# Performance work log

Measured on AMD Instinct MI355X. Metric: run time of the kernel, lower is better.

Reference implementation:

```python
import jax, jax.numpy as jnp
import numpy as np

N_NODES, N_EDGES, N_GRAPHS = 5000, 80000, 64
LATENT, HID, STEPS = 128, 512, 3


def _mlp(h, Ws, bs):
    # MLP: ReLU after every linear (incl. last) -- MLPwoLastAct is the variant without it
    for W, b in zip(Ws, bs):
        h = jax.nn.relu(h @ W + b)
    return h


def _mlp_wo_last_act(h, Ws, bs):
    n = len(Ws)
    for i, (W, b) in enumerate(zip(Ws, bs)):
        h = h @ W + b
        if i < n - 1:
            h = jax.nn.relu(h)
    return h


def setup_inputs() -> dict:
    key = jax.random.key(0)
    ks = iter(jax.random.split(key, 64))

    def nrm(shape, s=0.05):
        return (jax.random.normal(next(ks), shape) * s).astype(jnp.float32)

    inp = {}
    inp["x"] = jax.random.normal(next(ks), (N_NODES, LATENT), jnp.float32)
    inp["edge_index"] = jax.random.randint(next(ks), (2, N_EDGES), 0, N_NODES, jnp.int32)
    inp["edge_attr"] = jax.random.normal(next(ks), (N_EDGES, LATENT), jnp.float32)
    inp["u"] = jax.random.normal(next(ks), (N_GRAPHS, LATENT), jnp.float32)
    inp["node_batch"] = jnp.sort(jax.random.randint(next(ks), (N_NODES,), 0, N_GRAPHS, jnp.int32))
    inp["edge_batch"] = jnp.sort(jax.random.randint(next(ks), (N_EDGES,), 0, N_GRAPHS, jnp.int32))
    inp["pos"] = jax.random.normal(next(ks), (N_NODES, 3), jnp.float32)
    inp["last_pos_init"] = jax.random.uniform(next(ks), (N_NODES, 3), jnp.float32, -1.0, 1.0)

    # PosEmbeddingwithMask: pos MLP(3->128->128), dis MLP(1->128->128)
    inp["pos_emb_W1"], inp["pos_emb_b1"] = nrm((3, LATENT)), nrm((LATENT,))
    inp["pos_emb_W2"], inp["pos_emb_b2"] = nrm((LATENT, LATENT)), nrm((LATENT,))
    inp["dis_W1"], inp["dis_b1"] = nrm((1, LATENT)), nrm((LATENT,))
    inp["dis_W2"], inp["dis_b2"] = nrm((LATENT, LATENT)), nrm((LATENT,))

    # per-layer edge / node MLPs: (4*latent) -> 512 -> 512 -> 128, stacked over STEPS
    cin = 4 * LATENT
    for pre in ("edge", "node"):
        inp[f"{pre}_W1"], inp[f"{pre}_b1"] = nrm((STEPS, cin, HID)), nrm((STEPS, HID))
        inp[f"{pre}_W2"], inp[f"{pre}_b2"] = nrm((STEPS, HID, HID)), nrm((STEPS, HID))
        inp[f"{pre}_W3"], inp[f"{pre}_b3"] = nrm((STEPS, HID, LATENT)), nrm((STEPS, LATENT))

    # global MLP only for layers 0..STEPS-2: (3*latent) -> 512 -> 512 -> 128
    gL, gin = STEPS - 1, 3 * LATENT
    inp["glob_W1"], inp["glob_b1"] = nrm((gL, gin, HID)), nrm((gL, HID))
    inp["glob_W2"], inp["glob_b2"] = nrm((gL, HID, HID)), nrm((gL, HID))
    inp["glob_W3"], inp["glob_b3"] = nrm((gL, HID, LATENT)), nrm((gL, LATENT))

    # shared pos_decoder: MLPwoLastAct(128 -> 128 -> 3)
    inp["dec_W1"], inp["dec_b1"] = nrm((LATENT, LATENT)), nrm((LATENT,))
    inp["dec_W2"], inp["dec_b2"] = nrm((LATENT, 3)), nrm((3,))
    return inp


def reference(x, edge_index, edge_attr, u, node_batch, edge_batch, pos, last_pos_init,
              pos_emb_W1, pos_emb_b1, pos_emb_W2, pos_emb_b2,
              dis_W1, dis_b1, dis_W2, dis_b2,
              edge_W1, edge_b1, edge_W2, edge_b2, edge_W3, edge_b3,
              node_W1, node_b1, node_W2, node_b2, node_W3, node_b3,
              glob_W1, glob_b1, glob_W2, glob_b2, glob_W3, glob_b3,
              dec_W1, dec_b1, dec_W2, dec_b2):
    src, dst = edge_index[0], edge_index[1]
    N = x.shape[0]
    counts = jnp.maximum(
        jax.ops.segment_sum(jnp.ones((N, 1), x.dtype), node_batch, N_GRAPHS), 1.0)

    def move2origin(p):
        mean = jax.ops.segment_sum(p, node_batch, N_GRAPHS) / counts
        return p - mean[node_batch]

    xs, es, us = x, edge_attr, u
    last_pos = last_pos_init  # pos_new_zeros.uniform_(-1, 1), materialized as input
    pos_preds = []
    for l in range(STEPS):
        p = last_pos  # mode='mol2conf': pos = last_pred
        # PosEmbeddingwithMask
        ex = xs + _mlp(p, (pos_emb_W1, pos_emb_W2), (pos_emb_b1, pos_emb_b2))
        length = jnp.linalg.norm(p[src] - p[dst], axis=-1, keepdims=True)  # [E,1]
        ee = es + _mlp(length, (dis_W1, dis_W2), (dis_b1, dis_b2))
        # edge update: gather -> MLP
        edge_in = jnp.concatenate([ex[src], ex[dst], ee, us[edge_batch]], axis=-1)
        e1 = _mlp(edge_in, (edge_W1[l], edge_W2[l], edge_W3[l]),
                  (edge_b1[l], edge_b2[l], edge_b3[l]))
        # scatter-reduce (sum) to nodes, then node MLP
        sent = jax.ops.segment_sum(e1, src, N)
        recv = jax.ops.segment_sum(e1, dst, N)
        node_in = jnp.concatenate([ex, sent, recv, us[node_batch]], axis=-1)
        x1 = _mlp(node_in, (node_W1[l], node_W2[l], node_W3[l]),
                  (node_b1[l], node_b2[l], node_b3[l]))
        # global update (None on last layer)
        if l < STEPS - 1:
            g_in = jnp.concatenate([us,
                                    jax.ops.segment_sum(x1, node_batch, N_GRAPHS),
                                    jax.ops.segment_sum(e1, edge_batch, N_GRAPHS)], axis=-1)
            u1 = _mlp(g_in, (glob_W1[l], glob_W2[l], glob_W3[l]),
                      (glob_b1[l], glob_b2[l], glob_b3[l]))
        else:
            u1 = us
        # residuals (dropout is identity in eval)
        xs, es, us = x1 + xs, e1 + es, u1 + us
        # pred_pos_residual=True
        delta = _mlp_wo_last_act(xs, (dec_W1, dec_W2), (dec_b1, dec_b2))
        last_pos = move2origin(last_pos + delta)
        pos_preds.append(last_pos)
    return xs, es, us, jnp.stack(pos_preds)
```

## Files before the change

kernel.cpp:

```cpp
#include <hip/hip_runtime.h>
#include <hip/hip_bf16.h>
#include <stdint.h>

#define NN 5000
#define NE 80000
#define NG 64
#define LAT 128
#define HIDN 512

typedef __hip_bfloat16 bf16;
typedef short short8 __attribute__((ext_vector_type(8)));
typedef float f32x4 __attribute__((ext_vector_type(4)));

__device__ __forceinline__ float b2f(bf16 v) { return __bfloat162float(v); }
__device__ __forceinline__ bf16 f2b(float v) { return __float2bfloat16(v); }
__device__ __forceinline__ short f2bs(float v) {
    bf16 b = __float2bfloat16(v);
    short s; __builtin_memcpy(&s, &b, 2); return s;
}

template<int MODE>
__global__ __launch_bounds__(256, 4)
void gemm64_kernel(const bf16* __restrict__ A, const bf16* __restrict__ Bt,
                   const float* __restrict__ bias,
                   const float* residf, const bf16* residb,
                   float* out_sf, bf16* out_sb, bf16* out_rb,
                   int M, int N, int nnt,
                   const int* __restrict__ g_src, const int* __restrict__ g_dst,
                   const int* __restrict__ g_eb,
                   const bf16* __restrict__ g_ex, const bf16* __restrict__ g_ee,
                   const bf16* __restrict__ g_us)
{
    constexpr int K = 512, NT = K / 64;
    __shared__ __align__(16) char lds[24576];

    const int tid  = threadIdx.x;
    const int lane = tid & 63;
    const int w    = tid >> 6;
    const int li   = lane & 15, grp = lane >> 4;
    const int wr   = w >> 1, wc = w & 1;

    const int nb  = gridDim.x;
    const int q   = nb >> 3, r = nb & 7;
    const int xcd = blockIdx.x & 7, jj = blockIdx.x >> 3;
    const int wg  = (xcd < r ? xcd * (q + 1) : r * (q + 1) + (xcd - r) * q) + jj;
    const int m0  = (wg / nnt) * 128;
    const int n0  = (wg % nnt) * 64;

    f32x4 acc[4][2];
#pragma unroll
    for (int m = 0; m < 4; ++m)
#pragma unroll
        for (int n = 0; n < 2; ++n)
            acc[m][n] = (f32x4){0.f, 0.f, 0.f, 0.f};

    int he[4], hs[4], hd[4], hb[4];
    if (MODE == 1) {
#pragma unroll
        for (int c = 0; c < 4; ++c) {
            const int p  = (tid + c * 256) * 16;
            const int qb = p ^ ((p >> 3) & 0x70);
            int e = m0 + (qb >> 7); if (e >= M) e = M - 1;
            he[c] = e;
            hs[c] = g_src[e]; hd[c] = g_dst[e]; hb[c] = g_eb[e];
        }
    }

    char* ldsA = lds;
    char* ldsB = lds + 16384;

    for (int t = 0; t < NT; ++t) {
#pragma unroll
        for (int c = 0; c < 4; ++c) {
            const int p  = (tid + c * 256) * 16;
            const int qb = p ^ ((p >> 3) & 0x70);
            const int row = qb >> 7;
            const int kk  = (qb & 127) >> 1;
            const bf16* srcp;
            if (MODE == 1) {
                const int seg = t >> 1;
                const int so  = ((t & 1) << 6) + kk;
                if (seg == 0)      srcp = g_ex + (size_t)hs[c] * LAT + so;
                else if (seg == 1) srcp = g_ex + (size_t)hd[c] * LAT + so;
                else if (seg == 2) srcp = g_ee + (size_t)he[c] * LAT + so;
                else               srcp = g_us + (size_t)hb[c] * LAT + so;
            } else {
                int rr = m0 + row; if (rr >= M) rr = M - 1;
                srcp = A + (size_t)rr * K + t * 64 + kk;
            }
            __builtin_amdgcn_global_load_lds(
                (__attribute__((address_space(1))) const void*)srcp,
                (__attribute__((address_space(3))) void*)(ldsA + p), 16, 0, 0);
        }
#pragma unroll
        for (int c = 0; c < 2; ++c) {
            const int p  = (tid + c * 256) * 16;
            const int qb = p ^ ((p >> 3) & 0x70);
            const int row = qb >> 7;
            const int kk  = (qb & 127) >> 1;
            const bf16* srcp = Bt + (size_t)(n0 + row) * K + t * 64 + kk;
            __builtin_amdgcn_global_load_lds(
                (__attribute__((address_space(1))) const void*)srcp,
                (__attribute__((address_space(3))) void*)(ldsB + p), 16, 0, 0);
        }
        __syncthreads();

        short8 af[4][2], bf[2][2];
#pragma unroll
        for (int m = 0; m < 4; ++m) {
            const int row = wr * 64 + m * 16 + li;
            const int xr  = (row & 7) << 4;
#pragma unroll
            for (int s = 0; s < 2; ++s)
                af[m][s] = *(const short8*)(ldsA +
                    ((row * 128 + s * 64 + grp * 16) ^ xr));
        }
#pragma unroll
        for (int n = 0; n < 2; ++n) {
            const int row = wc * 32 + n * 16 + li;
            const int xr  = (row & 7) << 4;
#pragma unroll
            for (int s = 0; s < 2; ++s)
                bf[n][s] = *(const short8*)(ldsB +
                    ((row * 128 + s * 64 + grp * 16) ^ xr));
        }
#pragma unroll
        for (int m = 0; m < 4; ++m)
#pragma unroll
            for (int n = 0; n < 2; ++n)
#pragma unroll
                for (int s = 0; s < 2; ++s)
                    acc[m][n] = __builtin_amdgcn_mfma_f32_16x16x32_bf16(
                        af[m][s], bf[n][s], acc[m][n], 0, 0, 0);
        __syncthreads();
    }

#pragma unroll
    for (int m = 0; m < 4; ++m) {
        const int growb = m0 + wr * 64 + m * 16 + grp * 4;
#pragma unroll
        for (int n = 0; n < 2; ++n) {
            const int gcol = n0 + wc * 32 + n * 16 + li;
            const float bv = bias[gcol];
#pragma unroll
            for (int j = 0; j < 4; ++j) {
                const int grow = growb + j;
                if (grow >= M) continue;
                float val = fmaxf(acc[m][n][j] + bv, 0.f);
                const size_t oo = (size_t)grow * N + gcol;
                if (out_rb) out_rb[oo] = f2b(val);
                float sum = val;
                if (residf) sum += residf[oo];
                if (residb) sum += b2f(residb[oo]);
                if (out_sf) out_sf[oo] = sum;
                if (out_sb) out_sb[oo] = f2b(sum);
            }
        }
    }
}

template<int K, int MODE>
__global__ __launch_bounds__(256)
void gemm_kernel(const bf16* __restrict__ A,
                 const bf16* __restrict__ Bt,
                 const float* __restrict__ bias,
                 const float* residf, const bf16* residb,
                 float* out_sf, bf16* out_sb, bf16* out_rb,
                 int M, int N, int nnt,
                 const int* __restrict__ g_src, const int* __restrict__ g_dst,
                 const float* __restrict__ lp,
                 const float* __restrict__ aW, const float* __restrict__ ab)
{
    constexpr bool HASA = (MODE == 0);
    __shared__ __align__(16) bf16 As[HASA ? 128 * 32 : 8];
    __shared__ __align__(16) bf16 Bs[128 * 32];
    const int tid  = threadIdx.x;
    const int lane = tid & 63;
    const int w    = tid >> 6;
    const int li   = lane & 15, grp = lane >> 4;
    const int wr   = w >> 1, wc = w & 1;

    const int nb  = gridDim.x;
    const int q   = nb >> 3, r = nb & 7;
    const int xcd = blockIdx.x & 7, jj = blockIdx.x >> 3;
    const int wg  = (xcd < r ? xcd * (q + 1) : r * (q + 1) + (xcd - r) * q) + jj;
    const int m0  = (wg / nnt) * 128;
    const int n0  = (wg % nnt) * 128;

    f32x4 acc[4][4];
#pragma unroll
    for (int m = 0; m < 4; ++m)
#pragma unroll
        for (int n = 0; n < 4; ++n)
            acc[m][n] = (f32x4){0.f, 0.f, 0.f, 0.f};

    float r0[4], r1[4], r2[4];
    if (MODE == 2) {
#pragma unroll
        for (int m = 0; m < 4; ++m) {
            int rr = m0 + wr * 64 + m * 16 + li; if (rr >= M) rr = M - 1;
            r0[m] = lp[rr * 3 + 0]; r1[m] = lp[rr * 3 + 1]; r2[m] = lp[rr * 3 + 2];
        }
    } else if (MODE == 3) {
#pragma unroll
        for (int m = 0; m < 4; ++m) {
            int rr = m0 + wr * 64 + m * 16 + li; if (rr >= M) rr = M - 1;
            const int s = g_src[rr], d = g_dst[rr];
            const float dx = lp[s*3+0] - lp[d*3+0];
            const float dy = lp[s*3+1] - lp[d*3+1];
            const float dz = lp[s*3+2] - lp[d*3+2];
            r0[m] = sqrtf(dx*dx + dy*dy + dz*dz);
        }
    }

    const int offBase = w * 1024 + lane * 16;

    for (int kt = 0; kt < K / 32; ++kt) {
        if (HASA) {
#pragma unroll
            for (int c = 0; c < 2; ++c) {
                const int off = offBase + c * 4096;
                const int rr_ = off >> 6;
                const int g   = (off >> 4) & 3;
                const int gl  = g ^ ((rr_ >> 1) & 3);
                int rr = m0 + rr_; if (rr >= M) rr = M - 1;
                const bf16* srcp = A + (size_t)rr * K + kt * 32 + gl * 8;
                __builtin_amdgcn_global_load_lds(
                    (__attribute__((address_space(1))) const void*)srcp,
                    (__attribute__((address_space(3))) void*)((char*)As + off),
                    16, 0, 0);
            }
        }
#pragma unroll
        for (int c = 0; c < 2; ++c) {
            const int off = offBase + c * 4096;
            const int rr_ = off >> 6;
            const int g   = (off >> 4) & 3;
            const int gl  = g ^ ((rr_ >> 1) & 3);
            const bf16* srcp = Bt + (size_t)(n0 + rr_) * K + kt * 32 + gl * 8;
            __builtin_amdgcn_global_load_lds(
                (__attribute__((address_space(1))) const void*)srcp,
                (__attribute__((address_space(3))) void*)((char*)Bs + off),
                16, 0, 0);
        }
        __syncthreads();

        short8 af[4], bfr[4];
        if (HASA) {
#pragma unroll
            for (int m = 0; m < 4; ++m) {
                const int rr_  = wr * 64 + m * 16 + li;
                const int boff = rr_ * 64 + ((grp * 16) ^ (((rr_ >> 1) & 3) << 4));
                af[m] = *(const short8*)((const char*)As + boff);
            }
        } else {
            const int kk0 = kt * 32 + grp * 8;
            float bb[8], w0[8], w1[8], w2[8];
            *(f32x4*)&bb[0] = *(const f32x4*)(ab + kk0);
            *(f32x4*)&bb[4] = *(const f32x4*)(ab + kk0 + 4);
            *(f32x4*)&w0[0] = *(const f32x4*)(aW + kk0);
            *(f32x4*)&w0[4] = *(const f32x4*)(aW + kk0 + 4);
            if (MODE == 2) {
                *(f32x4*)&w1[0] = *(const f32x4*)(aW + K + kk0);
                *(f32x4*)&w1[4] = *(const f32x4*)(aW + K + kk0 + 4);
                *(f32x4*)&w2[0] = *(const f32x4*)(aW + 2 * K + kk0);
                *(f32x4*)&w2[4] = *(const f32x4*)(aW + 2 * K + kk0 + 4);
            }
#pragma unroll
            for (int m = 0; m < 4; ++m) {
                short8 v;
#pragma unroll
                for (int e = 0; e < 8; ++e) {
                    float s;
                    if (MODE == 2)
                        s = bb[e] + r0[m]*w0[e] + r1[m]*w1[e] + r2[m]*w2[e];
                    else
                        s = bb[e] + r0[m]*w0[e];
                    v[e] = f2bs(fmaxf(s, 0.f));
                }
                af[m] = v;
            }
        }
#pragma unroll
        for (int n = 0; n < 4; ++n) {
            const int rr_  = wc * 64 + n * 16 + li;
            const int boff = rr_ * 64 + ((grp * 16) ^ (((rr_ >> 1) & 3) << 4));
            bfr[n] = *(const short8*)((const char*)Bs + boff);
        }
#pragma unroll
        for (int m = 0; m < 4; ++m)
#pragma unroll
            for (int n = 0; n < 4; ++n)
                acc[m][n] = __builtin_amdgcn_mfma_f32_16x16x32_bf16(
                    af[m], bfr[n], acc[m][n], 0, 0, 0);
        __syncthreads();
    }

#pragma unroll
    for (int m = 0; m < 4; ++m) {
        const int growb = m0 + wr * 64 + m * 16 + grp * 4;
#pragma unroll
        for (int n = 0; n < 4; ++n) {
            const int gcol = n0 + wc * 64 + n * 16 + li;
            const float bv = bias[gcol];
#pragma unroll
            for (int j = 0; j < 4; ++j) {
                const int grow = growb + j;
                if (grow >= M) continue;
                float val = fmaxf(acc[m][n][j] + bv, 0.f);
                const size_t oo = (size_t)grow * N + gcol;
                if (out_rb) out_rb[oo] = f2b(val);
                float sum = val;
                if (residf) sum += residf[oo];
                if (residb) sum += b2f(residb[oo]);
                if (out_sf) out_sf[oo] = sum;
                if (out_sb) out_sb[oo] = f2b(sum);
            }
        }
    }
}

struct TDesc { const float* src; bf16* dst; int K, N, nblk, nb32; };
struct TPack { TDesc d[28]; int n; };

__global__ __launch_bounds__(256)
void transpose_kernel(TPack p)
{
    __shared__ float t[32][33];
    int b = blockIdx.x, mi = 0;
    while (mi < p.n && b >= p.d[mi].nblk) { b -= p.d[mi].nblk; ++mi; }
    if (mi >= p.n) return;
    TDesc d = p.d[mi];
    const int kb = b / d.nb32, nb = b % d.nb32;
    const int k0 = kb * 32, n0 = nb * 32;
    const int tx = threadIdx.x & 31, ty = threadIdx.x >> 5;
#pragma unroll
    for (int qq = 0; qq < 4; ++qq) {
        const int kk = ty + qq * 8;
        t[kk][tx] = d.src[(size_t)(k0 + kk) * d.N + n0 + tx];
    }
    __syncthreads();
#pragma unroll
    for (int qq = 0; qq < 4; ++qq) {
        const int nn = ty + qq * 8;
        d.dst[(size_t)(n0 + nn) * d.K + k0 + tx] = f2b(t[tx][nn]);
    }
}

__global__ void deg_kernel(const int* __restrict__ idx, int n, int* deg)
{
    int e = blockIdx.x * 256 + threadIdx.x;
    if (e < n) atomicAdd(&deg[idx[e]], 1);
}

__global__ __launch_bounds__(256)
void scan_kernel(const int* __restrict__ deg, int* __restrict__ offs, int n)
{
    __shared__ int tot[256];
    const int t = threadIdx.x;
    const int per = (n + 255) / 256;
    const int b = t * per;
    int s = 0;
    for (int i = 0; i < per; ++i) if (b + i < n) s += deg[b + i];
    tot[t] = s;
    __syncthreads();
    for (int d = 1; d < 256; d <<= 1) {
        int v = (t >= d) ? tot[t - d] : 0;
        __syncthreads();
        tot[t] += v;
        __syncthreads();
    }
    int excl = (t == 0) ? 0 : tot[t - 1];
    for (int i = 0; i < per; ++i)
        if (b + i < n) { offs[b + i] = excl; excl += deg[b + i]; }
    if (t == 255) offs[n] = tot[255];
}

__global__ void perm_kernel(const int* __restrict__ idx, int n,
                            int* cursor, int* __restrict__ perm)
{
    int e = blockIdx.x * 256 + threadIdx.x;
    if (e < n) { int p = atomicAdd(&cursor[idx[e]], 1); perm[p] = e; }
}

__global__ __launch_bounds__(128)
void node_in_kernel(const bf16* __restrict__ exb, const bf16* __restrict__ e1f,
                    const bf16* __restrict__ usb, const int* __restrict__ nbat,
                    const int* __restrict__ offs_s, const int* __restrict__ perm_s,
                    const int* __restrict__ offs_d, const int* __restrict__ perm_d,
                    bf16* __restrict__ node_in)
{
    const int i = blockIdx.x;
    const int c = threadIdx.x;
    float s1 = 0.f, s2 = 0.f;
    const int s_lo = offs_s[i], s_hi = offs_s[i + 1];
    for (int j = s_lo; j < s_hi; ++j)
        s1 += b2f(e1f[(size_t)perm_s[j] * LAT + c]);
    const int d_lo = offs_d[i], d_hi = offs_d[i + 1];
    for (int j = d_lo; j < d_hi; ++j)
        s2 += b2f(e1f[(size_t)perm_d[j] * LAT + c]);
    const size_t o = (size_t)i * (4 * LAT);
    node_in[o + c]           = exb[(size_t)i * LAT + c];
    node_in[o + LAT + c]     = f2b(s1);
    node_in[o + 2 * LAT + c] = f2b(s2);
    node_in[o + 3 * LAT + c] = usb[(size_t)nbat[i] * LAT + c];
}

__global__ __launch_bounds__(128)
void seg_reduce_kernel(const bf16* __restrict__ vals, const int* __restrict__ batch,
                       float* out, int R, int rows_per_block)
{
    const int r0 = blockIdx.x * rows_per_block;
    if (r0 >= R) return;
    const int c = threadIdx.x;
    const int r1 = min(r0 + rows_per_block, R);
    int g = batch[r0];
    float s = 0.f;
    for (int r = r0; r < r1; ++r) {
        const int gb = batch[r];
        if (gb != g) {
            atomicAdd(&out[(size_t)g * LAT + c], s);
            g = gb; s = 0.f;
        }
        s += b2f(vals[(size_t)r * LAT + c]);
    }
    atomicAdd(&out[(size_t)g * LAT + c], s);
}

__global__ void build_g_in_kernel(const float* __restrict__ us,
                                  const float* __restrict__ gx,
                                  const float* __restrict__ ge,
                                  bf16* __restrict__ out)
{
    int id = blockIdx.x * 256 + threadIdx.x;
    if (id >= NG * 384) return;
    int g = id / 384, c = id % 384;
    int seg = c >> 7, c7 = c & 127;
    float v;
    if (seg == 0)      v = us[g * LAT + c7];
    else if (seg == 1) v = gx[g * LAT + c7];
    else               v = ge[g * LAT + c7];
    out[id] = f2b(v);
}

__global__ void counts_kernel(const int* __restrict__ nbat, float* counts)
{
    int id = blockIdx.x * 256 + threadIdx.x;
    if (id < NN) atomicAdd(&counts[nbat[id]], 1.0f);
}

__global__ void cvt_kernel(const float* __restrict__ in, bf16* __restrict__ out, int n)
{
    int id = blockIdx.x * 256 + threadIdx.x;
    if (id < n) out[id] = f2b(in[id]);
}

__global__ void us_double_kernel(float* us)
{
    int id = blockIdx.x * 256 + threadIdx.x;
    if (id < NG * LAT) us[id] *= 2.0f;
}

__global__ __launch_bounds__(64)
void dec2_kernel(const bf16* __restrict__ dh, const float* __restrict__ W2,
                 const float* __restrict__ b2, const float* __restrict__ lp,
                 const int* __restrict__ nbat, float* __restrict__ ptmp, float* psum)
{
    int i = blockIdx.x;
    int l = threadIdx.x;
    float a0 = 0.f, a1 = 0.f, a2 = 0.f;
#pragma unroll
    for (int q = 0; q < 2; ++q) {
        int k = l + q * 64;
        float h = b2f(dh[i * LAT + k]);
        a0 += h * W2[k * 3 + 0];
        a1 += h * W2[k * 3 + 1];
        a2 += h * W2[k * 3 + 2];
    }
#pragma unroll
    for (int off = 32; off > 0; off >>= 1) {
        a0 += __shfl_down(a0, off, 64);
        a1 += __shfl_down(a1, off, 64);
        a2 += __shfl_down(a2, off, 64);
    }
    if (l == 0) {
        int g = nbat[i];
        float p0 = lp[i*3+0] + a0 + b2[0];
        float p1 = lp[i*3+1] + a1 + b2[1];
        float p2 = lp[i*3+2] + a2 + b2[2];
        ptmp[i*3+0] = p0; ptmp[i*3+1] = p1; ptmp[i*3+2] = p2;
        atomicAdd(&psum[g*3+0], p0);
        atomicAdd(&psum[g*3+1], p1);
        atomicAdd(&psum[g*3+2], p2);
    }
}

__global__ void finalize_pos_kernel(const float* __restrict__ ptmp,
                                    const float* __restrict__ psum,
                                    const float* __restrict__ counts,
                                    const int* __restrict__ nbat,
                                    float* __restrict__ lp, float* __restrict__ pos_out)
{
    int id = blockIdx.x * 256 + threadIdx.x;
    if (id >= NN * 3) return;
    int i = id / 3, d = id % 3;
    int g = nbat[i];
    float v = ptmp[id] - psum[g*3+d] / fmaxf(counts[g], 1.f);
    lp[id] = v;
    pos_out[id] = v;
}

extern "C" void kernel_launch(void* const* d_in, const int* in_sizes, int n_in,
                              void* d_out, int out_size, void* d_ws, size_t ws_size,
                              hipStream_t stream)
{
    const float* x        = (const float*)d_in[0];
    const int*   ei       = (const int*)d_in[1];
    const int*   src      = ei;
    const int*   dst      = ei + NE;
    const float* eattr    = (const float*)d_in[2];
    const float* u        = (const float*)d_in[3];
    const int*   nbat     = (const int*)d_in[4];
    const int*   ebat     = (const int*)d_in[5];
    const float* lp_init  = (const float*)d_in[7];
    const float* pW1 = (const float*)d_in[8];  const float* pb1 = (const float*)d_in[9];
    const float* pW2 = (const float*)d_in[10]; const float* pb2 = (const float*)d_in[11];
    const float* dW1 = (const float*)d_in[12]; const float* db1 = (const float*)d_in[13];
    const float* dW2 = (const float*)d_in[14]; const float* db2 = (const float*)d_in[15];
    const float* eW1 = (const float*)d_in[16]; const float* eb1 = (const float*)d_in[17];
    const float* eW2 = (const float*)d_in[18]; const float* eb2 = (const float*)d_in[19];
    const float* eW3 = (const float*)d_in[20]; const float* eb3 = (const float*)d_in[21];
    const float* nW1 = (const float*)d_in[22]; const float* nb1 = (const float*)d_in[23];
    const float* nW2 = (const float*)d_in[24]; const float* nb2 = (const float*)d_in[25];
    const float* nW3 = (const float*)d_in[26]; const float* nb3 = (const float*)d_in[27];
    const float* gW1 = (const float*)d_in[28]; const float* gb1 = (const float*)d_in[29];
    const float* gW2 = (const float*)d_in[30]; const float* gb2 = (const float*)d_in[31];
    const float* gW3 = (const float*)d_in[32]; const float* gb3 = (const float*)d_in[33];
    const float* dcW1 = (const float*)d_in[34]; const float* dcb1 = (const float*)d_in[35];
    const float* dcW2 = (const float*)d_in[36]; const float* dcb2 = (const float*)d_in[37];

    float* xs = (float*)d_out;
    float* es = xs + (size_t)NN * LAT;
    float* us = es + (size_t)NE * LAT;
    float* pos_out = us + (size_t)NG * LAT;

    char* wp = (char*)d_ws;
    auto alloc = [&](size_t nbytes) {
        void* r = (void*)wp;
        wp += (nbytes + 255) & ~(size_t)255;
        return r;
    };
    bf16* eW1t = (bf16*)alloc((size_t)3*512*512*2);
    bf16* eW2t = (bf16*)alloc((size_t)3*512*512*2);
    bf16* eW3t = (bf16*)alloc((size_t)3*128*512*2);
    bf16* nW1t = (bf16*)alloc((size_t)3*512*512*2);
    bf16* nW2t = (bf16*)alloc((size_t)3*512*512*2);
    bf16* nW3t = (bf16*)alloc((size_t)3*128*512*2);
    bf16* gW1t = (bf16*)alloc((size_t)2*512*384*2);
    bf16* gW2t = (bf16*)alloc((size_t)2*512*512*2);
    bf16* gW3t = (bf16*)alloc((size_t)2*128*512*2);
    bf16* pW2t = (bf16*)alloc((size_t)128*128*2);
    bf16* dW2t = (bf16*)alloc((size_t)128*128*2);
    bf16* dcW1t = (bf16*)alloc((size_t)128*128*2);
    bf16* exb  = (bf16*)alloc((size_t)NN*LAT*2);
    bf16* usb  = (bf16*)alloc((size_t)NG*LAT*2);
    bf16* esb  = (bf16*)alloc((size_t)NE*LAT*2);
    bf16* eeb  = (bf16*)alloc((size_t)NE*LAT*2);
    bf16* h1   = (bf16*)alloc((size_t)NE*HIDN*2);
    bf16* h2   = (bf16*)alloc((size_t)NE*HIDN*2);
    bf16* e1f  = (bf16*)alloc((size_t)NE*LAT*2);
    bf16* x1f  = (bf16*)alloc((size_t)NN*LAT*2);
    float* gx  = (float*)alloc((size_t)NG*LAT*4);
    float* ge  = (float*)alloc((size_t)NG*LAT*4);
    bf16* node_in = (bf16*)alloc((size_t)NN*HIDN*2);
    bf16* nh1  = (bf16*)alloc((size_t)NN*HIDN*2);
    bf16* nh2  = (bf16*)alloc((size_t)NN*HIDN*2);
    bf16* xsb  = (bf16*)alloc((size_t)NN*LAT*2);
    bf16* g_in = (bf16*)alloc((size_t)NG*384*2);
    bf16* gh1  = (bf16*)alloc((size_t)NG*HIDN*2);
    bf16* gh2  = (bf16*)alloc((size_t)NG*HIDN*2);
    bf16* dh   = (bf16*)alloc((size_t)NN*LAT*2);
    float* lp   = (float*)alloc((size_t)NN*3*4);
    float* ptmp = (float*)alloc((size_t)NN*3*4);
    float* psum = (float*)alloc((size_t)NG*3*4);
    float* counts = (float*)alloc((size_t)NG*4);
    int* deg    = (int*)alloc((size_t)NN*4);
    int* offs_s = (int*)alloc((size_t)(NN+1)*4);
    int* offs_d = (int*)alloc((size_t)(NN+1)*4);
    int* cur_s  = (int*)alloc((size_t)NN*4);
    int* cur_d  = (int*)alloc((size_t)NN*4);
    int* perm_s = (int*)alloc((size_t)NE*4);
    int* perm_d = (int*)alloc((size_t)NE*4);

    hipMemcpyAsync(xs, x,     (size_t)NN*LAT*4, hipMemcpyDeviceToDevice, stream);
    hipMemcpyAsync(us, u,     (size_t)NG*LAT*4, hipMemcpyDeviceToDevice, stream);
    hipMemcpyAsync(lp, lp_init, (size_t)NN*3*4, hipMemcpyDeviceToDevice, stream);
    hipMemsetAsync(counts, 0, NG*4, stream);
    counts_kernel<<<(NN+255)/256, 256, 0, stream>>>(nbat, counts);
    cvt_kernel<<<(NG*LAT+255)/256, 256, 0, stream>>>(us, usb, NG*LAT);
    cvt_kernel<<<(NE*LAT+255)/256, 256, 0, stream>>>(eattr, esb, NE*LAT);

    const int eb256 = (NE + 255) / 256;
    hipMemsetAsync(deg, 0, NN*4, stream);
    deg_kernel<<<eb256, 256, 0, stream>>>(src, NE, deg);
    scan_kernel<<<1, 256, 0, stream>>>(deg, offs_s, NN);
    hipMemsetAsync(deg, 0, NN*4, stream);
    deg_kernel<<<eb256, 256, 0, stream>>>(dst, NE, deg);
    scan_kernel<<<1, 256, 0, stream>>>(deg, offs_d, NN);
    hipMemcpyAsync(cur_s, offs_s, NN*4, hipMemcpyDeviceToDevice, stream);
    hipMemcpyAsync(cur_d, offs_d, NN*4, hipMemcpyDeviceToDevice, stream);
    perm_kernel<<<eb256, 256, 0, stream>>>(src, NE, cur_s, perm_s);
    perm_kernel<<<eb256, 256, 0, stream>>>(dst, NE, cur_d, perm_d);

    TPack pk{}; int nd = 0, totb = 0;
    auto addT = [&](const float* s, bf16* d, int K, int N) {
        pk.d[nd].src = s; pk.d[nd].dst = d; pk.d[nd].K = K; pk.d[nd].N = N;
        pk.d[nd].nblk = (K/32)*(N/32); pk.d[nd].nb32 = N/32;
        totb += pk.d[nd].nblk; ++nd;
    };
    for (int l = 0; l < 3; ++l) {
        addT(eW1 + (size_t)l*512*512, eW1t + (size_t)l*512*512, 512, 512);
        addT(eW2 + (size_t)l*512*512, eW2t + (size_t)l*512*512, 512, 512);
        addT(eW3 + (size_t)l*512*128, eW3t + (size_t)l*128*512, 512, 128);
        addT(nW1 + (size_t)l*512*512, nW1t + (size_t)l*512*512, 512, 512);
        addT(nW2 + (size_t)l*512*512, nW2t + (size_t)l*512*512, 512, 512);
        addT(nW3 + (size_t)l*512*128, nW3t + (size_t)l*128*512, 512, 128);
    }
    for (int l = 0; l < 2; ++l) {
        addT(gW1 + (size_t)l*384*512, gW1t + (size_t)l*512*384, 384, 512);
        addT(gW2 + (size_t)l*512*512, gW2t + (size_t)l*512*512, 512, 512);
        addT(gW3 + (size_t)l*512*128, gW3t + (size_t)l*128*512, 512, 128);
    }
    addT(pW2, pW2t, 128, 128);
    addT(dW2, dW2t, 128, 128);
    addT(dcW1, dcW1t, 128, 128);
    pk.n = nd;
    transpose_kernel<<<totb, 256, 0, stream>>>(pk);

    const int mtE  = NE / 128;
    const int mtN  = (NN + 127) / 128;
    #define NIL3 nullptr, nullptr, nullptr

    for (int l = 0; l < 3; ++l) {
        gemm_kernel<128,2><<<mtN, 256, 0, stream>>>(
            nullptr, pW2t, pb2, xs, nullptr, nullptr, exb, nullptr, NN, LAT, 1,
            nullptr, nullptr, lp, pW1, pb1);
        gemm_kernel<128,3><<<mtE, 256, 0, stream>>>(
            nullptr, dW2t, db2, nullptr, esb, nullptr, eeb, nullptr, NE, LAT, 1,
            src, dst, lp, dW1, db1);
        gemm64_kernel<1><<<mtE*8, 256, 0, stream>>>(
            nullptr, eW1t + (size_t)l*512*512, eb1 + l*HIDN, nullptr, nullptr,
            nullptr, nullptr, h1, NE, HIDN, 8,
            src, dst, ebat, exb, eeb, usb);
        gemm64_kernel<0><<<mtE*8, 256, 0, stream>>>(
            h1, eW2t + (size_t)l*512*512, eb2 + l*HIDN, nullptr, nullptr,
            nullptr, nullptr, h2, NE, HIDN, 8, NIL3, NIL3);
        gemm64_kernel<0><<<mtE*2, 256, 0, stream>>>(
            h2, eW3t + (size_t)l*128*512, eb3 + l*LAT, nullptr, esb,
            (l == 2 ? es : nullptr), (l < 2 ? esb : nullptr), e1f, NE, LAT, 2,
            NIL3, NIL3);
        if (l < 2) {
            hipMemsetAsync(gx, 0, (size_t)2*NG*LAT*4, stream);
            seg_reduce_kernel<<<(NE+63)/64, 128, 0, stream>>>(e1f, ebat, ge, NE, 64);
        }
        node_in_kernel<<<NN, 128, 0, stream>>>(
            exb, e1f, usb, nbat, offs_s, perm_s, offs_d, perm_d, node_in);
        gemm64_kernel<0><<<mtN*8, 256, 0, stream>>>(
            node_in, nW1t + (size_t)l*512*512, nb1 + l*HIDN, nullptr, nullptr,
            nullptr, nullptr, nh1, NN, HIDN, 8, NIL3, NIL3);
        gemm64_kernel<0><<<mtN*8, 256, 0, stream>>>(
            nh1, nW2t + (size_t)l*512*512, nb2 + l*HIDN, nullptr, nullptr,
            nullptr, nullptr, nh2, NN, HIDN, 8, NIL3, NIL3);
        gemm64_kernel<0><<<mtN*2, 256, 0, stream>>>(
            nh2, nW3t + (size_t)l*128*512, nb3 + l*LAT, xs, nullptr,
            xs, xsb, x1f, NN, LAT, 2, NIL3, NIL3);
        if (l < 2) {
            seg_reduce_kernel<<<(NN+31)/32, 128, 0, stream>>>(x1f, nbat, gx, NN, 32);
            build_g_in_kernel<<<(NG*384+255)/256, 256, 0, stream>>>(us, gx, ge, g_in);
            gemm_kernel<384,0><<<4, 256, 0, stream>>>(
                g_in, gW1t + (size_t)l*512*384, gb1 + l*HIDN, nullptr, nullptr,
                nullptr, nullptr, gh1, NG, HIDN, 4, NIL3, nullptr, nullptr);
            gemm_kernel<512,0><<<4, 256, 0, stream>>>(
                gh1, gW2t + (size_t)l*512*512, gb2 + l*HIDN, nullptr, nullptr,
                nullptr, nullptr, gh2, NG, HIDN, 4, NIL3, nullptr, nullptr);
            gemm_kernel<512,0><<<1, 256, 0, stream>>>(
                gh2, gW3t + (size_t)l*128*512, gb3 + l*LAT, us, nullptr,
                us, usb, nullptr, NG, LAT, 1, NIL3, nullptr, nullptr);
        } else {
            us_double_kernel<<<(NG*LAT+255)/256, 256, 0, stream>>>(us);
        }
        gemm_kernel<128,0><<<mtN, 256, 0, stream>>>(
            xsb, dcW1t, dcb1, nullptr, nullptr, nullptr, nullptr, dh, NN, LAT, 1,
            NIL3, nullptr, nullptr);
        hipMemsetAsync(psum, 0, NG*3*4, stream);
        dec2_kernel<<<NN, 64, 0, stream>>>(dh, dcW2, dcb2, lp, nbat, ptmp, psum);
        finalize_pos_kernel<<<(NN*3+255)/256, 256, 0, stream>>>(
            ptmp, psum, counts, nbat, lp, pos_out + (size_t)l*NN*3);
    }
    (void)in_sizes; (void)n_in; (void)out_size; (void)ws_size;
}
```

Baseline: 1.442 ms.

## Fuse pos/dis embeddings into one launch, merge edge segment reduce, halve GEMM N-tile

```diff
diff --git a/kernel.cpp b/kernel.cpp
--- a/kernel.cpp
+++ b/kernel.cpp
@@ -159,53 +159,50 @@
     }
 }
 
-template<int K, int MODE>
-__global__ __launch_bounds__(256)
-void gemm_kernel(const bf16* __restrict__ A,
-                 const bf16* __restrict__ Bt,
-                 const float* __restrict__ bias,
-                 const float* residf, const bf16* residb,
-                 float* out_sf, bf16* out_sb, bf16* out_rb,
-                 int M, int N, int nnt,
-                 const int* __restrict__ g_src, const int* __restrict__ g_dst,
-                 const float* __restrict__ lp,
-                 const float* __restrict__ aW, const float* __restrict__ ab)
-{
-    constexpr bool HASA = (MODE == 0);
-    __shared__ __align__(16) bf16 As[HASA ? 128 * 32 : 8];
-    __shared__ __align__(16) bf16 Bs[128 * 32];
+__global__ __launch_bounds__(256, 4)
+void posdis_kernel(int nP,
+                   const float* __restrict__ lp,
+                   const int* __restrict__ src, const int* __restrict__ dst,
+                   const bf16* __restrict__ pBt, const float* __restrict__ pb2v,
+                   const float* __restrict__ pW1v, const float* __restrict__ pb1v,
+                   const float* __restrict__ xs, bf16* __restrict__ exb,
+                   const bf16* __restrict__ dBt, const float* __restrict__ db2v,
+                   const float* __restrict__ dW1v, const float* __restrict__ db1v,
+                   const bf16* __restrict__ esb, bf16* __restrict__ eeb)
+{
+    constexpr int K = 128;
+    __shared__ __align__(16) bf16 Bs[64 * 32];
     const int tid  = threadIdx.x;
     const int lane = tid & 63;
     const int w    = tid >> 6;
     const int li   = lane & 15, grp = lane >> 4;
     const int wr   = w >> 1, wc = w & 1;
 
-    const int nb  = gridDim.x;
-    const int q   = nb >> 3, r = nb & 7;
-    const int xcd = blockIdx.x & 7, jj = blockIdx.x >> 3;
-    const int wg  = (xcd < r ? xcd * (q + 1) : r * (q + 1) + (xcd - r) * q) + jj;
-    const int m0  = (wg / nnt) * 128;
-    const int n0  = (wg % nnt) * 128;
-
-    f32x4 acc[4][4];
+    const bool isP = (int)blockIdx.x < nP;
+    const int bid  = isP ? blockIdx.x : blockIdx.x - nP;
+    const int M    = isP ? NN : NE;
+    const int m0   = (bid >> 1) * 128;
+    const int n0   = (bid & 1) * 64;
+    const bf16*  Bt   = isP ? pBt  : dBt;
+    const float* bias = isP ? pb2v : db2v;
+    const float* aW   = isP ? pW1v : dW1v;
+    const float* ab   = isP ? pb1v : db1v;
+
+    f32x4 acc[4][2];
 #pragma unroll
     for (int m = 0; m < 4; ++m)
 #pragma unroll
-        for (int n = 0; n < 4; ++n)
+        for (int n = 0; n < 2; ++n)
             acc[m][n] = (f32x4){0.f, 0.f, 0.f, 0.f};
 
     float r0[4], r1[4], r2[4];
-    if (MODE == 2) {
-#pragma unroll
-        for (int m = 0; m < 4; ++m) {
-            int rr = m0 + wr * 64 + m * 16 + li; if (rr >= M) rr = M - 1;
+#pragma unroll
+    for (int m = 0; m < 4; ++m) {
+        int rr = m0 + wr * 64 + m * 16 + li; if (rr >= M) rr = M - 1;
+        if (isP) {
             r0[m] = lp[rr * 3 + 0]; r1[m] = lp[rr * 3 + 1]; r2[m] = lp[rr * 3 + 2];
-        }
-    } else if (MODE == 3) {
-#pragma unroll
-        for (int m = 0; m < 4; ++m) {
-            int rr = m0 + wr * 64 + m * 16 + li; if (rr >= M) rr = M - 1;
-            const int s = g_src[rr], d = g_dst[rr];
+        } else {
+            const int s = src[rr], d = dst[rr];
             const float dx = lp[s*3+0] - lp[d*3+0];
             const float dy = lp[s*3+1] - lp[d*3+1];
             const float dz = lp[s*3+2] - lp[d*3+2];
@@ -213,27 +210,9 @@
         }
     }
 
-    const int offBase = w * 1024 + lane * 16;
-
     for (int kt = 0; kt < K / 32; ++kt) {
-        if (HASA) {
-#pragma unroll
-            for (int c = 0; c < 2; ++c) {
-                const int off = offBase + c * 4096;
-                const int rr_ = off >> 6;
-                const int g   = (off >> 4) & 3;
-                const int gl  = g ^ ((rr_ >> 1) & 3);
-                int rr = m0 + rr_; if (rr >= M) rr = M - 1;
-                const bf16* srcp = A + (size_t)rr * K + kt * 32 + gl * 8;
-                __builtin_amdgcn_global_load_lds(
-                    (__attribute__((address_space(1))) const void*)srcp,
-                    (__attribute__((address_space(3))) void*)((char*)As + off),
-                    16, 0, 0);
-            }
-        }
-#pragma unroll
-        for (int c = 0; c < 2; ++c) {
-            const int off = offBase + c * 4096;
+        {
+            const int off = tid * 16;
             const int rr_ = off >> 6;
             const int g   = (off >> 4) & 3;
             const int gl  = g ^ ((rr_ >> 1) & 3);
@@ -245,52 +224,40 @@
         }
         __syncthreads();
 
-        short8 af[4], bfr[4];
-        if (HASA) {
-#pragma unroll
-            for (int m = 0; m < 4; ++m) {
-                const int rr_  = wr * 64 + m * 16 + li;
-                const int boff = rr_ * 64 + ((grp * 16) ^ (((rr_ >> 1) & 3) << 4));
-                af[m] = *(const short8*)((const char*)As + boff);
+        const int kk0 = kt * 32 + grp * 8;
+        float bb[8], w0[8], w1[8], w2[8];
+        *(f32x4*)&bb[0] = *(const f32x4*)(ab + kk0);
+        *(f32x4*)&bb[4] = *(const f32x4*)(ab + kk0 + 4);
+        *(f32x4*)&w0[0] = *(const f32x4*)(aW + kk0);
+        *(f32x4*)&w0[4] = *(const f32x4*)(aW + kk0 + 4);
+        if (isP) {
+            *(f32x4*)&w1[0] = *(const f32x4*)(aW + K + kk0);
+            *(f32x4*)&w1[4] = *(const f32x4*)(aW + K + kk0 + 4);
+            *(f32x4*)&w2[0] = *(const f32x4*)(aW + 2 * K + kk0);
+            *(f32x4*)&w2[4] = *(const f32x4*)(aW + 2 * K + kk0 + 4);
+        }
+        short8 af[4], bfr[2];
+#pragma unroll
+        for (int m = 0; m < 4; ++m) {
+            short8 v;
+#pragma unroll
+            for (int e = 0; e < 8; ++e) {
+                float s = isP ? (bb[e] + r0[m]*w0[e] + r1[m]*w1[e] + r2[m]*w2[e])
+                              : (bb[e] + r0[m]*w0[e]);
+                v[e] = f2bs(fmaxf(s, 0.f));
             }
-        } else {
-            const int kk0 = kt * 32 + grp * 8;
-            float bb[8], w0[8], w1[8], w2[8];
-            *(f32x4*)&bb[0] = *(const f32x4*)(ab + kk0);
-            *(f32x4*)&bb[4] = *(const f32x4*)(ab + kk0 + 4);
-            *(f32x4*)&w0[0] = *(const f32x4*)(aW + kk0);
-            *(f32x4*)&w0[4] = *(const f32x4*)(aW + kk0 + 4);
-            if (MODE == 2) {
-                *(f32x4*)&w1[0] = *(const f32x4*)(aW + K + kk0);
-                *(f32x4*)&w1[4] = *(const f32x4*)(aW + K + kk0 + 4);
-                *(f32x4*)&w2[0] = *(const f32x4*)(aW + 2 * K + kk0);
-                *(f32x4*)&w2[4] = *(const f32x4*)(aW + 2 * K + kk0 + 4);
-            }
-#pragma unroll
-            for (int m = 0; m < 4; ++m) {
-                short8 v;
-#pragma unroll
-                for (int e = 0; e < 8; ++e) {
-                    float s;
-                    if (MODE == 2)
-                        s = bb[e] + r0[m]*w0[e] + r1[m]*w1[e] + r2[m]*w2[e];
-                    else
-                        s = bb[e] + r0[m]*w0[e];
-                    v[e] = f2bs(fmaxf(s, 0.f));
-                }
-                af[m] = v;
-            }
-        }
-#pragma unroll
-        for (int n = 0; n < 4; ++n) {
-            const int rr_  = wc * 64 + n * 16 + li;
+            af[m] = v;
+        }
+#pragma unroll
+        for (int n = 0; n < 2; ++n) {
+            const int rr_  = wc * 32 + n * 16 + li;
             const int boff = rr_ * 64 + ((grp * 16) ^ (((rr_ >> 1) & 3) << 4));
             bfr[n] = *(const short8*)((const char*)Bs + boff);
         }
 #pragma unroll
         for (int m = 0; m < 4; ++m)
 #pragma unroll
-            for (int n = 0; n < 4; ++n)
+            for (int n = 0; n < 2; ++n)
                 acc[m][n] = __builtin_amdgcn_mfma_f32_16x16x32_bf16(
                     af[m], bfr[n], acc[m][n], 0, 0, 0);
         __syncthreads();
@@ -300,8 +267,110 @@
     for (int m = 0; m < 4; ++m) {
         const int growb = m0 + wr * 64 + m * 16 + grp * 4;
 #pragma unroll
-        for (int n = 0; n < 4; ++n) {
-            const int gcol = n0 + wc * 64 + n * 16 + li;
+        for (int n = 0; n < 2; ++n) {
+            const int gcol = n0 + wc * 32 + n * 16 + li;
+            const float bv = bias[gcol];
+#pragma unroll
+            for (int j = 0; j < 4; ++j) {
+                const int grow = growb + j;
+                if (grow >= M) continue;
+                float val = fmaxf(acc[m][n][j] + bv, 0.f);
+                const size_t oo = (size_t)grow * LAT + gcol;
+                if (isP) exb[oo] = f2b(val + xs[oo]);
+                else     eeb[oo] = f2b(val + b2f(esb[oo]));
+            }
+        }
+    }
+}
+
+template<int K>
+__global__ __launch_bounds__(256, 4)
+void gemm_kernel(const bf16* __restrict__ A,
+                 const bf16* __restrict__ Bt,
+                 const float* __restrict__ bias,
+                 const float* residf,
+                 float* out_sf, bf16* out_sb, bf16* out_rb,
+                 int M, int N, int nnt)
+{
+    __shared__ __align__(16) bf16 As[128 * 32];
+    __shared__ __align__(16) bf16 Bs[64 * 32];
+    const int tid  = threadIdx.x;
+    const int lane = tid & 63;
+    const int w    = tid >> 6;
+    const int li   = lane & 15, grp = lane >> 4;
+    const int wr   = w >> 1, wc = w & 1;
+
+    const int nb  = gridDim.x;
+    const int q   = nb >> 3, r = nb & 7;
+    const int xcd = blockIdx.x & 7, jj = blockIdx.x >> 3;
+    const int wg  = (nb >= 8)
+        ? (xcd < r ? xcd * (q + 1) : r * (q + 1) + (xcd - r) * q) + jj
+        : (int)blockIdx.x;
+    const int m0  = (wg / nnt) * 128;
+    const int n0  = (wg % nnt) * 64;
+
+    f32x4 acc[4][2];
+#pragma unroll
+    for (int m = 0; m < 4; ++m)
+#pragma unroll
+        for (int n = 0; n < 2; ++n)
+            acc[m][n] = (f32x4){0.f, 0.f, 0.f, 0.f};
+
+    for (int kt = 0; kt < K / 32; ++kt) {
+#pragma unroll
+        for (int c = 0; c < 2; ++c) {
+            const int off = tid * 16 + c * 4096;
+            const int rr_ = off >> 6;
+            const int g   = (off >> 4) & 3;
+            const int gl  = g ^ ((rr_ >> 1) & 3);
+            int rr = m0 + rr_; if (rr >= M) rr = M - 1;
+            const bf16* srcp = A + (size_t)rr * K + kt * 32 + gl * 8;
+            __builtin_amdgcn_global_load_lds(
+                (__attribute__((address_space(1))) const void*)srcp,
+                (__attribute__((address_space(3))) void*)((char*)As + off),
+                16, 0, 0);
+        }
+        {
+            const int off = tid * 16;
+            const int rr_ = off >> 6;
+            const int g   = (off >> 4) & 3;
+            const int gl  = g ^ ((rr_ >> 1) & 3);
+            const bf16* srcp = Bt + (size_t)(n0 + rr_) * K + kt * 32 + gl * 8;
+            __builtin_amdgcn_global_load_lds(
+                (__attribute__((address_space(1))) const void*)srcp,
+                (__attribute__((address_space(3))) void*)((char*)Bs + off),
+                16, 0, 0);
+        }
+        __syncthreads();
+
+        short8 af[4], bfr[2];
+#pragma unroll
+        for (int m = 0; m < 4; ++m) {
+            const int rr_  = wr * 64 + m * 16 + li;
+            const int boff = rr_ * 64 + ((grp * 16) ^ (((rr_ >> 1) & 3) << 4));
+            af[m] = *(const short8*)((const char*)As + boff);
+        }
+#pragma unroll
+        for (int n = 0; n < 2; ++n) {
+            const int rr_  = wc * 32 + n * 16 + li;
+            const int boff = rr_ * 64 + ((grp * 16) ^ (((rr_ >> 1) & 3) << 4));
+            bfr[n] = *(const short8*)((const char*)Bs + boff);
+        }
+#pragma unroll
+        for (int m = 0; m < 4; ++m)
+#pragma unroll
+            for (int n = 0; n < 2; ++n)
+                acc[m][n] = __builtin_amdgcn_mfma_f32_16x16x32_bf16(
+                    af[m], bfr[n], acc[m][n], 0, 0, 0);
+        __syncthreads();
+    }
+
+#pragma unroll
+    for (int m = 0; m < 4; ++m) {
+        const int growb = m0 + wr * 64 + m * 16 + grp * 4;
+#pragma unroll
+        for (int n = 0; n < 2; ++n) {
+            const int gcol = n0 + wc * 32 + n * 16 + li;
             const float bv = bias[gcol];
 #pragma unroll
             for (int j = 0; j < 4; ++j) {
@@ -312,7 +381,6 @@
                 if (out_rb) out_rb[oo] = f2b(val);
                 float sum = val;
                 if (residf) sum += residf[oo];
-                if (residb) sum += b2f(residb[oo]);
                 if (out_sf) out_sf[oo] = sum;
                 if (out_sb) out_sb[oo] = f2b(sum);
             }
@@ -384,14 +452,32 @@
 }
 
 __global__ __launch_bounds__(128)
-void node_in_kernel(const bf16* __restrict__ exb, const bf16* __restrict__ e1f,
-                    const bf16* __restrict__ usb, const int* __restrict__ nbat,
-                    const int* __restrict__ offs_s, const int* __restrict__ perm_s,
-                    const int* __restrict__ offs_d, const int* __restrict__ perm_d,
-                    bf16* __restrict__ node_in)
-{
+void node_seg_kernel(const bf16* __restrict__ exb, const bf16* __restrict__ e1f,
+                     const bf16* __restrict__ usb, const int* __restrict__ nbat,
+                     const int* __restrict__ offs_s, const int* __restrict__ perm_s,
+                     const int* __restrict__ offs_d, const int* __restrict__ perm_d,
+                     bf16* __restrict__ node_in,
+                     const int* __restrict__ ebat, float* ge)
+{
+    const int c = threadIdx.x;
+    if ((int)blockIdx.x >= NN) {
+        const int r0 = ((int)blockIdx.x - NN) * 64;
+        if (r0 >= NE) return;
+        const int r1 = min(r0 + 64, NE);
+        int g = ebat[r0];
+        float s = 0.f;
+        for (int r = r0; r < r1; ++r) {
+            const int gb = ebat[r];
+            if (gb != g) {
+                atomicAdd(&ge[(size_t)g * LAT + c], s);
+                g = gb; s = 0.f;
+            }
+            s += b2f(e1f[(size_t)r * LAT + c]);
+        }
+        atomicAdd(&ge[(size_t)g * LAT + c], s);
+        return;
+    }
     const int i = blockIdx.x;
-    const int c = threadIdx.x;
     float s1 = 0.f, s2 = 0.f;
     const int s_lo = offs_s[i], s_hi = offs_s[i + 1];
     for (int j = s_lo; j < s_hi; ++j)
@@ -642,12 +728,10 @@
     #define NIL3 nullptr, nullptr, nullptr
 
     for (int l = 0; l < 3; ++l) {
-        gemm_kernel<128,2><<<mtN, 256, 0, stream>>>(
-            nullptr, pW2t, pb2, xs, nullptr, nullptr, exb, nullptr, NN, LAT, 1,
-            nullptr, nullptr, lp, pW1, pb1);
-        gemm_kernel<128,3><<<mtE, 256, 0, stream>>>(
-            nullptr, dW2t, db2, nullptr, esb, nullptr, eeb, nullptr, NE, LAT, 1,
-            src, dst, lp, dW1, db1);
+        posdis_kernel<<<mtN*2 + mtE*2, 256, 0, stream>>>(
+            mtN*2, lp, src, dst,
+            pW2t, pb2, pW1, pb1, xs, exb,
+            dW2t, db2, dW1, db1, esb, eeb);
         gemm64_kernel<1><<<mtE*8, 256, 0, stream>>>(
             nullptr, eW1t + (size_t)l*512*512, eb1 + l*HIDN, nullptr, nullptr,
             nullptr, nullptr, h1, NE, HIDN, 8,
@@ -659,12 +743,11 @@
             h2, eW3t + (size_t)l*128*512, eb3 + l*LAT, nullptr, esb,
             (l == 2 ? es : nullptr), (l < 2 ? esb : nullptr), e1f, NE, LAT, 2,
             NIL3, NIL3);
-        if (l < 2) {
+        if (l < 2)
             hipMemsetAsync(gx, 0, (size_t)2*NG*LAT*4, stream);
-            seg_reduce_kernel<<<(NE+63)/64, 128, 0, stream>>>(e1f, ebat, ge, NE, 64);
-        }
-        node_in_kernel<<<NN, 128, 0, stream>>>(
-            exb, e1f, usb, nbat, offs_s, perm_s, offs_d, perm_d, node_in);
+        node_seg_kernel<<<NN + (l < 2 ? (NE+63)/64 : 0), 128, 0, stream>>>(
+            exb, e1f, usb, nbat, offs_s, perm_s, offs_d, perm_d, node_in,
+            ebat, ge);
         gemm64_kernel<0><<<mtN*8, 256, 0, stream>>>(
             node_in, nW1t + (size_t)l*512*512, nb1 + l*HIDN, nullptr, nullptr,
             nullptr, nullptr, nh1, NN, HIDN, 8, NIL3, NIL3);
@@ -677,21 +760,20 @@
         if (l < 2) {
             seg_reduce_kernel<<<(NN+31)/32, 128, 0, stream>>>(x1f, nbat, gx, NN, 32);
             build_g_in_kernel<<<(NG*384+255)/256, 256, 0, stream>>>(us, gx, ge, g_in);
-            gemm_kernel<384,0><<<4, 256, 0, stream>>>(
-                g_in, gW1t + (size_t)l*512*384, gb1 + l*HIDN, nullptr, nullptr,
-                nullptr, nullptr, gh1, NG, HIDN, 4, NIL3, nullptr, nullptr);
-            gemm_kernel<512,0><<<4, 256, 0, stream>>>(
-                gh1, gW2t + (size_t)l*512*512, gb2 + l*HIDN, nullptr, nullptr,
-                nullptr, nullptr, gh2, NG, HIDN, 4, NIL3, nullptr, nullptr);
-            gemm_kernel<512,0><<<1, 256, 0, stream>>>(
-                gh2, gW3t + (size_t)l*128*512, gb3 + l*LAT, us, nullptr,
-                us, usb, nullptr, NG, LAT, 1, NIL3, nullptr, nullptr);
+            gemm_kernel<384><<<8, 256, 0, stream>>>(
+                g_in, gW1t + (size_t)l*512*384, gb1 + l*HIDN, nullptr,
+                nullptr, nullptr, gh1, NG, HIDN, 8);
+            gemm_kernel<512><<<8, 256, 0, stream>>>(
+                gh1, gW2t + (size_t)l*512*512, gb2 + l*HIDN, nullptr,
+                nullptr, nullptr, gh2, NG, HIDN, 8);
+            gemm_kernel<512><<<2, 256, 0, stream>>>(
+                gh2, gW3t + (size_t)l*128*512, gb3 + l*LAT, us,
+                us, usb, nullptr, NG, LAT, 2);
         } else {
             us_double_kernel<<<(NG*LAT+255)/256, 256, 0, stream>>>(us);
         }
-        gemm_kernel<128,0><<<mtN, 256, 0, stream>>>(
-            xsb, dcW1t, dcb1, nullptr, nullptr, nullptr, nullptr, dh, NN, LAT, 1,
-            NIL3, nullptr, nullptr);
+        gemm_kernel<128><<<mtN*2, 256, 0, stream>>>(
+            xsb, dcW1t, dcb1, nullptr, nullptr, nullptr, dh, NN, LAT, 2);
         hipMemsetAsync(psum, 0, NG*3*4, stream);
         dec2_kernel<<<NN, 64, 0, stream>>>(dh, dcW2, dcb2, lp, nbat, ptmp, psum);
         finalize_pos_kernel<<<(NN*3+255)/256, 256, 0, stream>>>(
```

New measurement: 1.277 ms (median of 2 runs). 1.13x faster.
